# Optimization experiments

Hardware: AMD Instinct MI355X
Metric: run time of the kernel (lower is better)

Reference implementation:

```python
import jax, jax.numpy as jnp
import numpy as np

B, C, F, T = 8, 64, 256, 512
CA = 5          # channel_attention
NTHR = 23       # number of threshold channels (loop breaks at i=24 where cnt hits 1.0)
BN_EPS = 1e-5

# thresholds: cnt accumulates i*(1/300) in python float -> cnt_i = i(i+1)/600
THRESHOLDS = jnp.asarray(np.cumsum(np.arange(1, NTHR + 1) / 300.0), dtype=jnp.float32)


def setup_inputs() -> dict:
    key = jax.random.key(0)
    ks = jax.random.split(key, 12)
    s = 0.05
    return {
        "feature_in": jax.random.normal(ks[0], (B, C, F, T), jnp.float32),
        "w1": jax.random.normal(ks[1], (CA, C), jnp.float32) * s,   # cov1d_d_1 weight [out,in] (k=1)
        "b1": jax.random.normal(ks[2], (CA,), jnp.float32) * s,
        "w2": jax.random.normal(ks[3], (C, CA), jnp.float32) * s,   # cov1d_d_2 weight
        "b2": jax.random.normal(ks[4], (C,), jnp.float32) * s,
        "wc": jax.random.normal(ks[5], (C,), jnp.float32) * s,      # conv2d_fn C->1, 1x1
        "bc": jax.random.normal(ks[6], (1,), jnp.float32) * s,
        "wc2": jax.random.normal(ks[7], (C, NTHR), jnp.float32) * s,  # conv2d_fn_2 23->C, 1x1
        "bc2": jax.random.normal(ks[8], (C,), jnp.float32) * s,
        "wo": jax.random.normal(ks[9], (C, 2 * C), jnp.float32) * s,  # out_conv2d 2C->C, 1x1
        "bo": jax.random.normal(ks[10], (C,), jnp.float32) * s,
        "gamma": jnp.ones((C,), jnp.float32),
        "beta": jnp.zeros((C,), jnp.float32),
    }


def _chan_mlp(z, w1, b1, w2, b2):
    # z: [B, C, L] -> sigmoid(conv1(relu(conv0(z)))) ; both convs are kernel-1 channel mixes
    h = jax.nn.relu(jnp.einsum('oc,bcl->bol', w1, z) + b1[None, :, None])
    return jax.nn.sigmoid(jnp.einsum('co,bol->bcl', w2, h) + b2[None, :, None])


def reference(feature_in, w1, b1, w2, b2, wc, bc, wc2, bc2, wo, bo, gamma, beta):
    # --- DTFA ---
    zt = _chan_mlp(jnp.mean(feature_in, axis=2), w1, b1, w2, b2)  # [B,C,T]
    zf = _chan_mlp(jnp.mean(feature_in, axis=3), w1, b1, w2, b2)  # [B,C,F]
    # matmul([B,C,F,1],[B,C,1,T]) == outer-product broadcast
    outer = zf[:, :, :, None] * zt[:, :, None, :]                 # [B,C,F,T]
    att_map = jnp.einsum('bcft,c->bft', outer, wc) + bc[0]        # [B,F,T] (squeezed 1-channel)
    # thresholded channel stack: channel i = att_map * (att_map > thr_i)
    dcomp = jnp.where(att_map[:, None] > THRESHOLDS[None, :, None, None],
                      att_map[:, None], 0.0)                      # [B,23,F,T]
    att = jnp.einsum('bkft,ck->bcft', dcomp, wc2) + bc2[None, :, None, None]
    att = att * feature_in                                        # [B,C,F,T]
    # --- block tail: concat -> 1x1 conv -> BN(train stats) -> ReLU ---
    concat = jnp.concatenate([feature_in, att], axis=1)           # [B,2C,F,T]
    o = jnp.einsum('bkft,ck->bcft', concat, wo) + bo[None, :, None, None]
    mu = jnp.mean(o, axis=(0, 2, 3), keepdims=True)
    var = jnp.var(o, axis=(0, 2, 3), keepdims=True)
    o = (o - mu) * jax.lax.rsqrt(var + BN_EPS)
    o = o * gamma[None, :, None, None] + beta[None, :, None, None]
    return jax.nn.relu(o)
```

## Files before the change

### kernel.cpp

```cpp
#include <hip/hip_runtime.h>

#define Bn 8
#define Cn 64
#define Fn 256
#define Tn 512
#define FT (Fn*Tn)
#define NPIX (Bn*Fn*Tn)
#define NTOT (Bn*Cn*Fn*Tn)

#define WS_MT    0
#define WS_MF    262144
#define WS_ZT    393216
#define WS_ZFW   655360
#define WS_P     786432
#define WS_THR   787968
#define WS_AHI   788000
#define WS_ALO   792096
#define WS_PSH   796192
#define WS_SCALE 804384
#define WS_SHIFT 804448

typedef __attribute__((ext_vector_type(8))) short bf16x8;
typedef __attribute__((ext_vector_type(4))) float f32x4;

__device__ __forceinline__ void split2(float x, unsigned short& h, unsigned short& l) {
    unsigned u = __builtin_bit_cast(unsigned, x);
    unsigned r = u + 0x7FFFu + ((u >> 16) & 1u);
    h = (unsigned short)(r >> 16);
    float hf = __builtin_bit_cast(float, r & 0xFFFF0000u);
    float lo = x - hf;
    unsigned ul = __builtin_bit_cast(unsigned, lo);
    unsigned rl = ul + 0x7FFFu + ((ul >> 16) & 1u);
    l = (unsigned short)(rl >> 16);
}

__global__ __launch_bounds__(256) void k1_sums(const float* __restrict__ x,
                                               float* __restrict__ ws) {
    const int bx = blockIdx.x;
    const int slab = bx >> 3, chunk = bx & 7;
    const int wave = threadIdx.x >> 6, lane = threadIdx.x & 63;
    const float4* x4 = (const float4*)x + (size_t)slab * (FT / 4) + chunk * 32 * 128;
    __shared__ float lcs[4 * 512];
    float4 cs0 = {0.f,0.f,0.f,0.f}, cs1 = {0.f,0.f,0.f,0.f};
    #pragma unroll
    for (int r = 0; r < 8; ++r) {
        const int row = wave * 8 + r;
        float4 v0 = x4[row * 128 + lane];
        float4 v1 = x4[row * 128 + 64 + lane];
        cs0.x += v0.x; cs0.y += v0.y; cs0.z += v0.z; cs0.w += v0.w;
        cs1.x += v1.x; cs1.y += v1.y; cs1.z += v1.z; cs1.w += v1.w;
        float rs = (v0.x + v0.y) + (v0.z + v0.w) + (v1.x + v1.y) + (v1.z + v1.w);
        #pragma unroll
        for (int m = 1; m < 64; m <<= 1) rs += __shfl_xor(rs, m, 64);
        if (lane == 0) ws[WS_MF + slab * Fn + chunk * 32 + row] = rs;
    }
    ((float4*)lcs)[wave * 128 + lane] = cs0;
    ((float4*)lcs)[wave * 128 + 64 + lane] = cs1;
    __syncthreads();
    for (int t = threadIdx.x; t < 512; t += 256) {
        float s = lcs[t] + lcs[512 + t] + lcs[1024 + t] + lcs[1536 + t];
        atomicAdd(&ws[WS_MT + slab * Tn + t], s);
    }
}

__global__ __launch_bounds__(256) void k2_mlp_prep(
    const float* __restrict__ w1, const float* __restrict__ b1,
    const float* __restrict__ w2, const float* __restrict__ b2,
    const float* __restrict__ wc, const float* __restrict__ bc2,
    const float* __restrict__ wo, const float* __restrict__ wc2,
    float* __restrict__ ws) {
    const int blk = blockIdx.x;
    if (blk < 1536) {
        const int wave = threadIdx.x >> 6, c = threadIdx.x & 63;
        const bool is_t = (blk < 1024);
        float m; int b, l;
        if (is_t) {
            const int p = blk * 4 + wave;
            b = p >> 9; l = p & 511;
            m = ws[WS_MT + (b * 64 + c) * Tn + l] * (1.0f / Fn);
        } else {
            const int p = (blk - 1024) * 4 + wave;
            b = p >> 8; l = p & 255;
            m = ws[WS_MF + (b * 64 + c) * Fn + l] * (1.0f / Tn);
        }
        float acc = b2[c];
        #pragma unroll
        for (int o = 0; o < 5; ++o) {
            float v = w1[o * 64 + c] * m;
            #pragma unroll
            for (int mm = 1; mm < 64; mm <<= 1) v += __shfl_xor(v, mm, 64);
            const float h = fmaxf(v + b1[o], 0.0f);
            acc = fmaf(w2[c * 5 + o], h, acc);
        }
        const float sg = 1.0f / (1.0f + expf(-acc));
        if (is_t) ws[WS_ZT  + (b * 64 + c) * Tn + l] = sg;
        else      ws[WS_ZFW + (b * 64 + c) * Fn + l] = sg * wc[c];
    } else {
        const int tid = threadIdx.x;
        unsigned short* AH = (unsigned short*)(ws + WS_AHI);
        unsigned short* AL = (unsigned short*)(ws + WS_ALO);
        for (int i = tid; i < 8192; i += 256) {
            const int chunk = i >> 9, within = i & 511;
            const int quad = within >> 7, m16 = (within >> 3) & 15, j = within & 7;
            const int m = (chunk & 3) * 16 + m16;
            const int k = (chunk >> 2) * 32 + quad * 8 + j;
            float v;
            if (k < 64) v = wo[m * 128 + k] + wo[m * 128 + 64 + k] * bc2[k];
            else        v = wo[m * 128 + k];
            unsigned short h, l;
            split2(v, h, l);
            AH[i] = h; AL[i] = l;
        }
        for (int c = tid; c < 64; c += 256) {
            float a = 0.f;
            ws[WS_P + c * 24 + 0] = 0.f;
            for (int K = 1; K <= 23; ++K) { a += wc2[c * 23 + K - 1]; ws[WS_P + c * 24 + K] = a; }
        }
        if (tid == 0) {
            double a = 0.0;
            for (int i = 1; i <= 23; ++i) { a += (double)i / 300.0; ws[WS_THR + i - 1] = (float)a; }
            for (int i = 23; i < 32; ++i) ws[WS_THR + i] = 1e30f;
        }
        for (int i = tid; i < 8192; i += 256) ws[WS_PSH + i] = 0.f;
    }
}

__global__ __launch_bounds__(256) void k4_main(
    const float* __restrict__ x, const float* __restrict__ wsc,
    const float* __restrict__ bc, const float* __restrict__ bo,
    float* __restrict__ out, float* __restrict__ ws) {
    __shared__ __align__(16) short Bhi[16 * 512];
    __shared__ __align__(16) short Blo[16 * 512];
    __shared__ float Pl[64 * 24];
    __shared__ float sstat[128];

    const int tid = threadIdx.x;
    const int blk = blockIdx.x;
    const int b = blk >> 11;
    const int rem = blk & 2047;
    const int f = rem >> 3;
    const int t0 = (rem & 7) << 6;

    for (int i = tid; i < 1536; i += 256) Pl[i] = wsc[WS_P + i];
    if (tid < 128) sstat[tid] = 0.f;

    const int t_local = tid & 63, kg = tid >> 6;
    const int t = t0 + t_local;
    const int nfrag = t_local >> 4, n16 = t_local & 15;

    const float* zfw = wsc + WS_ZFW + b * (Cn * Fn) + f;
    const float* zt  = wsc + WS_ZT  + b * (Cn * Tn) + t;
    float am = bc[0];
    #pragma unroll
    for (int c = 0; c < 64; ++c) am = fmaf(zfw[c * Fn], zt[c * Tn], am);
    int L = 0;
    #pragma unroll
    for (int i = 0; i < 23; ++i) L += (am > wsc[WS_THR + i]) ? 1 : 0;

    __syncthreads();

    const float* xb = x + (size_t)b * (Cn * FT) + f * Tn + t;
    #pragma unroll
    for (int g = 0; g < 2; ++g) {
        const int k8 = (kg + g * 4) << 3;
        float xv[8];
        #pragma unroll
        for (int i = 0; i < 8; ++i) xv[i] = xb[(size_t)(k8 + i) * FT];
        unsigned ph[4], pl[4];
        #pragma unroll
        for (int i = 0; i < 4; ++i) {
            unsigned short h0, l0, h1, l1;
            split2(xv[2 * i], h0, l0); split2(xv[2 * i + 1], h1, l1);
            ph[i] = (unsigned)h0 | ((unsigned)h1 << 16);
            pl[i] = (unsigned)l0 | ((unsigned)l1 << 16);
        }
        const int cka = ((k8 >> 5) * 4 + nfrag) * 512 + ((k8 >> 3) & 3) * 128 + n16 * 8;
        *(int4*)&Bhi[cka] = make_int4(ph[0], ph[1], ph[2], ph[3]);
        *(int4*)&Blo[cka] = make_int4(pl[0], pl[1], pl[2], pl[3]);
        float gv[8];
        #pragma unroll
        for (int i = 0; i < 8; ++i) gv[i] = am * Pl[(k8 + i) * 24 + L] * xv[i];
        #pragma unroll
        for (int i = 0; i < 4; ++i) {
            unsigned short h0, l0, h1, l1;
            split2(gv[2 * i], h0, l0); split2(gv[2 * i + 1], h1, l1);
            ph[i] = (unsigned)h0 | ((unsigned)h1 << 16);
            pl[i] = (unsigned)l0 | ((unsigned)l1 << 16);
        }
        *(int4*)&Bhi[cka + 4096] = make_int4(ph[0], ph[1], ph[2], ph[3]);
        *(int4*)&Blo[cka + 4096] = make_int4(pl[0], pl[1], pl[2], pl[3]);
    }
    __syncthreads();

    const int lane = tid & 63, w = tid >> 6;
    const int quad = lane >> 4, l16 = lane & 15;
    const short* AH = (const short*)(wsc + WS_AHI);
    const short* AL = (const short*)(wsc + WS_ALO);

    f32x4 acc[4];
    const float4 bo4 = *(const float4*)&bo[w * 16 + quad * 4];
    #pragma unroll
    for (int nf = 0; nf < 4; ++nf) { acc[nf].x = bo4.x; acc[nf].y = bo4.y; acc[nf].z = bo4.z; acc[nf].w = bo4.w; }

    #pragma unroll
    for (int ks = 0; ks < 4; ++ks) {
        const int ao = (ks * 4 + w) * 512 + quad * 128 + l16 * 8;
        const bf16x8 ah = *(const bf16x8*)(AH + ao);
        const bf16x8 al = *(const bf16x8*)(AL + ao);
        #pragma unroll
        for (int nf = 0; nf < 4; ++nf) {
            const int bof = (ks * 4 + nf) * 512 + quad * 128 + l16 * 8;
            const bf16x8 bh = *(const bf16x8*)&Bhi[bof];
            const bf16x8 bl = *(const bf16x8*)&Blo[bof];
            acc[nf] = __builtin_amdgcn_mfma_f32_16x16x32_bf16(ah, bh, acc[nf], 0, 0, 0);
            acc[nf] = __builtin_amdgcn_mfma_f32_16x16x32_bf16(ah, bl, acc[nf], 0, 0, 0);
            acc[nf] = __builtin_amdgcn_mfma_f32_16x16x32_bf16(al, bh, acc[nf], 0, 0, 0);
        }
    }

    float* ob = out + (size_t)b * (Cn * FT) + f * Tn + t0;
    #pragma unroll
    for (int r = 0; r < 4; ++r) {
        const int c = w * 16 + quad * 4 + r;
        float vs = 0.f, vq = 0.f;
        #pragma unroll
        for (int nf = 0; nf < 4; ++nf) {
            const float v = acc[nf][r];
            ob[(size_t)c * FT + nf * 16 + l16] = v;
            vs += v; vq = fmaf(v, v, vq);
        }
        #pragma unroll
        for (int m = 1; m < 16; m <<= 1) { vs += __shfl_xor(vs, m); vq += __shfl_xor(vq, m); }
        if (l16 == 0) { sstat[c] = vs; sstat[64 + c] = vq; }
    }
    __syncthreads();
    if (tid < 128) atomicAdd(&ws[WS_PSH + (blk & 63) * 128 + tid], sstat[tid]);
}

__global__ void k6_fin(const float* __restrict__ gamma, const float* __restrict__ beta,
                       float* __restrict__ ws) {
    const int c = threadIdx.x;
    if (c < 64) {
        float s = 0.f, q = 0.f;
        for (int sh = 0; sh < 64; ++sh) {
            s += ws[WS_PSH + sh * 128 + c];
            q += ws[WS_PSH + sh * 128 + 64 + c];
        }
        const float n = (float)NPIX;
        const float mu = s / n;
        const float var = q / n - mu * mu;
        const float sc = gamma[c] * rsqrtf(var + 1e-5f);
        ws[WS_SCALE + c] = sc;
        ws[WS_SHIFT + c] = beta[c] - mu * sc;
    }
}

__global__ __launch_bounds__(256) void k7_norm(float* __restrict__ o,
                                               const float* __restrict__ ws) {
    const int blk = blockIdx.x;
    const int slab = blk >> 5, chunk = blk & 31;
    const int c = slab & 63;
    const float sc = ws[WS_SCALE + c], sh = ws[WS_SHIFT + c];
    float4* o4 = (float4*)o + (size_t)slab * (FT / 4) + chunk * 1024;
    #pragma unroll
    for (int i = 0; i < 4; ++i) {
        float4 v = o4[i * 256 + threadIdx.x];
        v.x = fmaxf(fmaf(v.x, sc, sh), 0.f);
        v.y = fmaxf(fmaf(v.y, sc, sh), 0.f);
        v.z = fmaxf(fmaf(v.z, sc, sh), 0.f);
        v.w = fmaxf(fmaf(v.w, sc, sh), 0.f);
        o4[i * 256 + threadIdx.x] = v;
    }
}

extern "C" void kernel_launch(void* const* d_in, const int* in_sizes, int n_in,
                              void* d_out, int out_size, void* d_ws, size_t ws_size,
                              hipStream_t stream) {
    const float* x     = (const float*)d_in[0];
    const float* w1    = (const float*)d_in[1];
    const float* b1    = (const float*)d_in[2];
    const float* w2    = (const float*)d_in[3];
    const float* b2    = (const float*)d_in[4];
    const float* wc    = (const float*)d_in[5];
    const float* bc    = (const float*)d_in[6];
    const float* wc2   = (const float*)d_in[7];
    const float* bc2   = (const float*)d_in[8];
    const float* wo    = (const float*)d_in[9];
    const float* bo    = (const float*)d_in[10];
    const float* gamma = (const float*)d_in[11];
    const float* beta  = (const float*)d_in[12];
    float* out = (float*)d_out;
    float* ws  = (float*)d_ws;

    hipMemsetAsync(ws + WS_MT, 0, Bn * Cn * Tn * sizeof(float), stream);
    k1_sums<<<4096, 256, 0, stream>>>(x, ws);
    k2_mlp_prep<<<1537, 256, 0, stream>>>(w1, b1, w2, b2, wc, bc2, wo, wc2, ws);
    k4_main<<<16384, 256, 0, stream>>>(x, ws, bc, bo, out, ws);
    k6_fin<<<1, 64, 0, stream>>>(gamma, beta, ws);
    k7_norm<<<16384, 256, 0, stream>>>(out, ws);
}
```

Measured before the change: 720.8 us.

## Drop lo-split for attention half, use hw bf16 pack, fold BN finalize into norm

```diff
diff --git a/kernel.cpp b/kernel.cpp
--- a/kernel.cpp
+++ b/kernel.cpp
@@ -32,6 +32,12 @@
     unsigned ul = __builtin_bit_cast(unsigned, lo);
     unsigned rl = ul + 0x7FFFu + ((ul >> 16) & 1u);
     l = (unsigned short)(rl >> 16);
+}
+
+__device__ __forceinline__ unsigned pk2(float a, float b) {
+    unsigned r;
+    asm("v_cvt_pk_bf16_f32 %0, %1, %2" : "=v"(r) : "v"(a), "v"(b));
+    return r;
 }
 
 __global__ __launch_bounds__(256) void k1_sums(const float* __restrict__ x,
@@ -125,13 +131,14 @@
     }
 }
 
-__global__ __launch_bounds__(256) void k4_main(
+__global__ __launch_bounds__(256, 5) void k4_main(
     const float* __restrict__ x, const float* __restrict__ wsc,
     const float* __restrict__ bc, const float* __restrict__ bo,
     float* __restrict__ out, float* __restrict__ ws) {
     __shared__ __align__(16) short Bhi[16 * 512];
-    __shared__ __align__(16) short Blo[16 * 512];
+    __shared__ __align__(16) short Blo[8 * 512];
     __shared__ float Pl[64 * 24];
+    __shared__ float AmP[4 * 64];
     __shared__ float sstat[128];
 
     const int tid = threadIdx.x;
@@ -141,54 +148,67 @@
     const int f = rem >> 3;
     const int t0 = (rem & 7) << 6;
 
-    for (int i = tid; i < 1536; i += 256) Pl[i] = wsc[WS_P + i];
-    if (tid < 128) sstat[tid] = 0.f;
-
     const int t_local = tid & 63, kg = tid >> 6;
     const int t = t0 + t_local;
     const int nfrag = t_local >> 4, n16 = t_local & 15;
 
+    const float* xb = x + (size_t)b * (Cn * FT) + f * Tn + t;
+    float xv[16];
+    #pragma unroll
+    for (int g = 0; g < 2; ++g) {
+        const int k8 = (kg + g * 4) << 3;
+        #pragma unroll
+        for (int i = 0; i < 8; ++i) xv[g * 8 + i] = xb[(size_t)(k8 + i) * FT];
+    }
+
+    for (int i = tid; i < 1536; i += 256) Pl[i] = wsc[WS_P + i];
+
     const float* zfw = wsc + WS_ZFW + b * (Cn * Fn) + f;
     const float* zt  = wsc + WS_ZT  + b * (Cn * Tn) + t;
-    float am = bc[0];
-    #pragma unroll
-    for (int c = 0; c < 64; ++c) am = fmaf(zfw[c * Fn], zt[c * Tn], am);
-    int L = 0;
-    #pragma unroll
-    for (int i = 0; i < 23; ++i) L += (am > wsc[WS_THR + i]) ? 1 : 0;
-
-    __syncthreads();
-
-    const float* xb = x + (size_t)b * (Cn * FT) + f * Tn + t;
+    float amp = 0.f;
+    #pragma unroll
+    for (int cc = 0; cc < 16; ++cc) {
+        const int c = kg * 16 + cc;
+        amp = fmaf(zfw[c * Fn], zt[c * Tn], amp);
+    }
+    AmP[kg * 64 + t_local] = amp;
+
     #pragma unroll
     for (int g = 0; g < 2; ++g) {
         const int k8 = (kg + g * 4) << 3;
-        float xv[8];
-        #pragma unroll
-        for (int i = 0; i < 8; ++i) xv[i] = xb[(size_t)(k8 + i) * FT];
         unsigned ph[4], pl[4];
         #pragma unroll
         for (int i = 0; i < 4; ++i) {
-            unsigned short h0, l0, h1, l1;
-            split2(xv[2 * i], h0, l0); split2(xv[2 * i + 1], h1, l1);
-            ph[i] = (unsigned)h0 | ((unsigned)h1 << 16);
-            pl[i] = (unsigned)l0 | ((unsigned)l1 << 16);
+            const float x0 = xv[g * 8 + 2 * i], x1 = xv[g * 8 + 2 * i + 1];
+            const unsigned h = pk2(x0, x1);
+            const float hf0 = __builtin_bit_cast(float, h << 16);
+            const float hf1 = __builtin_bit_cast(float, h & 0xFFFF0000u);
+            ph[i] = h;
+            pl[i] = pk2(x0 - hf0, x1 - hf1);
         }
         const int cka = ((k8 >> 5) * 4 + nfrag) * 512 + ((k8 >> 3) & 3) * 128 + n16 * 8;
         *(int4*)&Bhi[cka] = make_int4(ph[0], ph[1], ph[2], ph[3]);
         *(int4*)&Blo[cka] = make_int4(pl[0], pl[1], pl[2], pl[3]);
-        float gv[8];
-        #pragma unroll
-        for (int i = 0; i < 8; ++i) gv[i] = am * Pl[(k8 + i) * 24 + L] * xv[i];
+    }
+    __syncthreads();
+
+    float am = bc[0] + AmP[t_local] + AmP[64 + t_local] + AmP[128 + t_local] + AmP[192 + t_local];
+    int L = 0;
+    #pragma unroll
+    for (int i = 0; i < 23; ++i) L += (am > wsc[WS_THR + i]) ? 1 : 0;
+
+    #pragma unroll
+    for (int g = 0; g < 2; ++g) {
+        const int k8 = (kg + g * 4) << 3;
+        unsigned pg[4];
         #pragma unroll
         for (int i = 0; i < 4; ++i) {
-            unsigned short h0, l0, h1, l1;
-            split2(gv[2 * i], h0, l0); split2(gv[2 * i + 1], h1, l1);
-            ph[i] = (unsigned)h0 | ((unsigned)h1 << 16);
-            pl[i] = (unsigned)l0 | ((unsigned)l1 << 16);
-        }
-        *(int4*)&Bhi[cka + 4096] = make_int4(ph[0], ph[1], ph[2], ph[3]);
-        *(int4*)&Blo[cka + 4096] = make_int4(pl[0], pl[1], pl[2], pl[3]);
+            const float g0 = am * Pl[(k8 + 2 * i)     * 24 + L] * xv[g * 8 + 2 * i];
+            const float g1 = am * Pl[(k8 + 2 * i + 1) * 24 + L] * xv[g * 8 + 2 * i + 1];
+            pg[i] = pk2(g0, g1);
+        }
+        const int cka = ((k8 >> 5) * 4 + nfrag) * 512 + ((k8 >> 3) & 3) * 128 + n16 * 8;
+        *(int4*)&Bhi[cka + 4096] = make_int4(pg[0], pg[1], pg[2], pg[3]);
     }
     __syncthreads();
 
@@ -211,9 +231,11 @@
         for (int nf = 0; nf < 4; ++nf) {
             const int bof = (ks * 4 + nf) * 512 + quad * 128 + l16 * 8;
             const bf16x8 bh = *(const bf16x8*)&Bhi[bof];
-            const bf16x8 bl = *(const bf16x8*)&Blo[bof];
             acc[nf] = __builtin_amdgcn_mfma_f32_16x16x32_bf16(ah, bh, acc[nf], 0, 0, 0);
-            acc[nf] = __builtin_amdgcn_mfma_f32_16x16x32_bf16(ah, bl, acc[nf], 0, 0, 0);
+            if (ks < 2) {
+                const bf16x8 bl = *(const bf16x8*)&Blo[bof];
+                acc[nf] = __builtin_amdgcn_mfma_f32_16x16x32_bf16(ah, bl, acc[nf], 0, 0, 0);
+            }
             acc[nf] = __builtin_amdgcn_mfma_f32_16x16x32_bf16(al, bh, acc[nf], 0, 0, 0);
         }
     }
@@ -237,39 +259,40 @@
     if (tid < 128) atomicAdd(&ws[WS_PSH + (blk & 63) * 128 + tid], sstat[tid]);
 }
 
-__global__ void k6_fin(const float* __restrict__ gamma, const float* __restrict__ beta,
-                       float* __restrict__ ws) {
-    const int c = threadIdx.x;
-    if (c < 64) {
+__global__ __launch_bounds__(256) void k7_norm(float* __restrict__ o,
+                                               const float* __restrict__ gamma,
+                                               const float* __restrict__ beta,
+                                               const float* __restrict__ ws) {
+    __shared__ float ssc[64], ssh[64];
+    const int tid = threadIdx.x;
+    if (tid < 64) {
         float s = 0.f, q = 0.f;
+        #pragma unroll 8
         for (int sh = 0; sh < 64; ++sh) {
-            s += ws[WS_PSH + sh * 128 + c];
-            q += ws[WS_PSH + sh * 128 + 64 + c];
+            s += ws[WS_PSH + sh * 128 + tid];
+            q += ws[WS_PSH + sh * 128 + 64 + tid];
         }
         const float n = (float)NPIX;
         const float mu = s / n;
         const float var = q / n - mu * mu;
-        const float sc = gamma[c] * rsqrtf(var + 1e-5f);
-        ws[WS_SCALE + c] = sc;
-        ws[WS_SHIFT + c] = beta[c] - mu * sc;
-    }
-}
-
-__global__ __launch_bounds__(256) void k7_norm(float* __restrict__ o,
-                                               const float* __restrict__ ws) {
+        const float sc = gamma[tid] * rsqrtf(var + 1e-5f);
+        ssc[tid] = sc;
+        ssh[tid] = beta[tid] - mu * sc;
+    }
+    __syncthreads();
     const int blk = blockIdx.x;
     const int slab = blk >> 5, chunk = blk & 31;
     const int c = slab & 63;
-    const float sc = ws[WS_SCALE + c], sh = ws[WS_SHIFT + c];
+    const float sc = ssc[c], sh = ssh[c];
     float4* o4 = (float4*)o + (size_t)slab * (FT / 4) + chunk * 1024;
     #pragma unroll
     for (int i = 0; i < 4; ++i) {
-        float4 v = o4[i * 256 + threadIdx.x];
+        float4 v = o4[i * 256 + tid];
         v.x = fmaxf(fmaf(v.x, sc, sh), 0.f);
         v.y = fmaxf(fmaf(v.y, sc, sh), 0.f);
         v.z = fmaxf(fmaf(v.z, sc, sh), 0.f);
         v.w = fmaxf(fmaf(v.w, sc, sh), 0.f);
-        o4[i * 256 + threadIdx.x] = v;
+        o4[i * 256 + tid] = v;
     }
 }
 
@@ -296,6 +319,5 @@
     k1_sums<<<4096, 256, 0, stream>>>(x, ws);
     k2_mlp_prep<<<1537, 256, 0, stream>>>(w1, b1, w2, b2, wc, bc2, wo, wc2, ws);
     k4_main<<<16384, 256, 0, stream>>>(x, ws, bc, bo, out, ws);
-    k6_fin<<<1, 64, 0, stream>>>(gamma, beta, ws);
-    k7_norm<<<16384, 256, 0, stream>>>(out, ws);
-}
+    k7_norm<<<16384, 256, 0, stream>>>(out, gamma, beta, ws);
+}
```

Result: faster. 686.2 us (-4.8%).
